# Performance work log

Hardware: AMD Instinct MI355X
Metric: run time of the kernel (lower is better)

## Reference

```python
import jax, jax.numpy as jnp
import numpy as np

B, D_IN, D_OUT, M, KS = 8192, 4096, 4096, 32, 256
CHUNK = D_IN // M  # 128; d_input divisible by m -> all chunks equal width


def setup_inputs() -> dict:
    key = jax.random.key(0)
    k1, k2, k3, k4 = jax.random.split(key, 4)
    x = jax.random.normal(k1, (B, D_IN), dtype=jnp.float32)
    W = jax.random.normal(k2, (M, CHUNK, KS), dtype=jnp.float32) * (1.0 / np.sqrt(CHUNK))
    b = jax.random.normal(k3, (M, KS), dtype=jnp.float32) * 0.01
    idx = jax.random.randint(k4, (M, D_OUT), 0, KS)
    return {"x": x, "W": W, "b": b, "idx": idx}


def reference(x, W, b, idx):
    # x: (B, d_input); W: (m, chunk, ks); b: (m, ks); idx: (m, d_output)
    Bn = x.shape[0]
    m, chunk, ks = W.shape
    d_out = idx.shape[1]
    xs = x.reshape(Bn, m, chunk)
    # All m small Linears as one batched GEMM -> (m, B, ks)
    proj = jnp.einsum('bmc,mck->mbk', xs, W) + b[:, None, :]
    # Gather per-chunk codebook outputs and accumulate without materializing (B, m, d_out)
    def step(acc, inputs):
        p, ix = inputs  # p: (B, ks), ix: (d_out,)
        return acc + p[:, ix], None
    init = jnp.zeros((Bn, d_out), dtype=x.dtype)
    out, _ = jax.lax.scan(step, init, (proj, idx))
    return out
```

## Files before the change

### kernel.cpp

```cpp
#include <hip/hip_runtime.h>
#include <cstdint>


#define M_CB   32
#define CHUNK_C 128
#define KS_K   256
#define DIN    4096

#define GLOAD_LDS16(gp, lp)                                                      \
  __builtin_amdgcn_global_load_lds(                                              \
      (const __attribute__((address_space(1))) void*)(gp),                       \
      (__attribute__((address_space(3))) void*)(lp), 16, 0, 0)

__global__ __launch_bounds__(256, 3)
void k1_gemm(const float* __restrict__ x, const float* __restrict__ W,
             const float* __restrict__ bias, float* __restrict__ proj,
             int b0_chunk, int Bc) {
  const int t  = threadIdx.x;
  const int bq = t & 15;
  const int g  = t >> 4;
  const int m  = blockIdx.y;
  const int bb = blockIdx.x * 64;

  __shared__ float xs[32 * 68];
  __shared__ float Wl[32 * 256];

  float4 acc[16];
#pragma unroll
  for (int a = 0; a < 4; ++a) {
    float4 bv = *(const float4*)&bias[m * KS_K + g * 16 + 4 * a];
    acc[4 * a + 0] = make_float4(bv.x, bv.x, bv.x, bv.x);
    acc[4 * a + 1] = make_float4(bv.y, bv.y, bv.y, bv.y);
    acc[4 * a + 2] = make_float4(bv.z, bv.z, bv.z, bv.z);
    acc[4 * a + 3] = make_float4(bv.w, bv.w, bv.w, bv.w);
  }

  const float* xg = x + (size_t)(b0_chunk + bb) * DIN + m * CHUNK_C;
  const float* Wg = W + (size_t)m * CHUNK_C * KS_K;

  for (int cc = 0; cc < 4; ++cc) {
    __syncthreads();
    {
      const float* src = Wg + (size_t)(cc * 32) * KS_K;
      const int wb = (t & ~63);
#pragma unroll
      for (int i = 0; i < 8; ++i) {
        const int C = t + 256 * i;
        GLOAD_LDS16(src + 4 * C, (char*)Wl + (size_t)(wb + 256 * i) * 16);
      }
    }
#pragma unroll
    for (int i = 0; i < 2; ++i) {
      const int f = t + 256 * i;
      const int b = f >> 3, cq = f & 7;
      float4 v = *(const float4*)&xg[(size_t)b * DIN + cc * 32 + 4 * cq];
      xs[(4 * cq + 0) * 68 + b] = v.x;
      xs[(4 * cq + 1) * 68 + b] = v.y;
      xs[(4 * cq + 2) * 68 + b] = v.z;
      xs[(4 * cq + 3) * 68 + b] = v.w;
    }
    asm volatile("s_waitcnt vmcnt(0)" ::: "memory");
    __syncthreads();

#define FMA4(J, S)                                      \
  {                                                     \
    acc[J].x = fmaf(xq.x, (S), acc[J].x);               \
    acc[J].y = fmaf(xq.y, (S), acc[J].y);               \
    acc[J].z = fmaf(xq.z, (S), acc[J].z);               \
    acc[J].w = fmaf(xq.w, (S), acc[J].w);               \
  }
#pragma unroll 2
    for (int c = 0; c < 32; ++c) {
      float4 xq = *(float4*)&xs[c * 68 + 4 * bq];
      float4 w0 = *(float4*)&Wl[c * 256 + g * 16 + 0];
      float4 w1 = *(float4*)&Wl[c * 256 + g * 16 + 4];
      float4 w2 = *(float4*)&Wl[c * 256 + g * 16 + 8];
      float4 w3 = *(float4*)&Wl[c * 256 + g * 16 + 12];
      FMA4(0, w0.x)  FMA4(1, w0.y)  FMA4(2, w0.z)  FMA4(3, w0.w)
      FMA4(4, w1.x)  FMA4(5, w1.y)  FMA4(6, w1.z)  FMA4(7, w1.w)
      FMA4(8, w2.x)  FMA4(9, w2.y)  FMA4(10, w2.z) FMA4(11, w2.w)
      FMA4(12, w3.x) FMA4(13, w3.y) FMA4(14, w3.z) FMA4(15, w3.w)
    }
#undef FMA4
  }

#pragma unroll
  for (int j = 0; j < 16; ++j) {
    const int k = g * 16 + j;
    *(float4*)&proj[((size_t)m * KS_K + k) * Bc + bb + 4 * bq] = acc[j];
  }
}

__global__ __launch_bounds__(512, 2)
void k2_gather(const float* __restrict__ proj, const int* __restrict__ idx,
               float* __restrict__ out, int b0_chunk, int Bc, int D_out) {
  const int t  = threadIdx.x;
  const int q  = t & 7;
  const int g  = t >> 3;
  const int b0 = blockIdx.x * 32;
  const int dbase = blockIdx.y * 2048 + g * 32;

  __shared__ float pb[2][8192];

  float4 acc[32];
#pragma unroll
  for (int j = 0; j < 32; ++j) acc[j] = make_float4(0.f, 0.f, 0.f, 0.f);

  const int q16 = q << 4;
  const int* ixp = idx + dbase;

#define STAGE(MM, BUF)                                                          \
  {                                                                             \
    const float* src_ = proj + (size_t)(MM)*KS_K * Bc + b0;                     \
    const int wb_ = (t & ~63);                                                  \
    _Pragma("unroll") for (int i_ = 0; i_ < 4; ++i_) {                          \
      const int C_ = t + 512 * i_;              \
      const int k_ = C_ >> 3, qp_ = C_ & 7;                                     \
      GLOAD_LDS16(src_ + (size_t)k_ * Bc + 4 * qp_,                             \
                  (char*)(BUF) + (size_t)(wb_ + 512 * i_) * 16);                \
    }                                                                           \
  }

  STAGE(0, pb[0]);
  int4 iv[8];
#pragma unroll
  for (int a = 0; a < 8; ++a) iv[a] = *(const int4*)&ixp[4 * a];
  asm volatile("s_waitcnt vmcnt(0)" ::: "memory");
  __syncthreads();

  int cur = 0;
  for (int m = 0; m < M_CB; ++m) {
    int4 ivn[8];
    if (m < M_CB - 1) {
      const int* ixn = ixp + (size_t)(m + 1) * D_out;
#pragma unroll
      for (int a = 0; a < 8; ++a) ivn[a] = *(const int4*)&ixn[4 * a];
      STAGE(m + 1, pb[cur ^ 1]);
    }

    const char* pbase = (const char*)&pb[cur][0] + q16;
#define GSTEP(KV, J)                                                            \
  {                                                                             \
    const float4 v_ = *(const float4*)(pbase + ((KV) << 7));                    \
    acc[J].x += v_.x; acc[J].y += v_.y; acc[J].z += v_.z; acc[J].w += v_.w;     \
  }
#pragma unroll
    for (int a = 0; a < 8; ++a) {
      GSTEP(iv[a].x, 4 * a + 0)
      GSTEP(iv[a].y, 4 * a + 1)
      GSTEP(iv[a].z, 4 * a + 2)
      GSTEP(iv[a].w, 4 * a + 3)
    }
#undef GSTEP
    asm volatile("s_waitcnt vmcnt(0)" ::: "memory");
    __syncthreads();
    if (m < M_CB - 1) {
#pragma unroll
      for (int a = 0; a < 8; ++a) iv[a] = ivn[a];
    }
    cur ^= 1;
  }
#undef STAGE

  float* op = out + (size_t)(b0_chunk + b0 + 4 * q) * D_out + dbase;
#pragma unroll
  for (int a = 0; a < 8; ++a) {
    float4 o0 = make_float4(acc[4*a+0].x, acc[4*a+1].x, acc[4*a+2].x, acc[4*a+3].x);
    float4 o1 = make_float4(acc[4*a+0].y, acc[4*a+1].y, acc[4*a+2].y, acc[4*a+3].y);
    float4 o2 = make_float4(acc[4*a+0].z, acc[4*a+1].z, acc[4*a+2].z, acc[4*a+3].z);
    float4 o3 = make_float4(acc[4*a+0].w, acc[4*a+1].w, acc[4*a+2].w, acc[4*a+3].w);
    *(float4*)(op + 0 * (size_t)D_out + 4 * a) = o0;
    *(float4*)(op + 1 * (size_t)D_out + 4 * a) = o1;
    *(float4*)(op + 2 * (size_t)D_out + 4 * a) = o2;
    *(float4*)(op + 3 * (size_t)D_out + 4 * a) = o3;
  }
}

extern "C" void kernel_launch(void* const* d_in, const int* in_sizes, int n_in,
                              void* d_out, int out_size, void* d_ws, size_t ws_size,
                              hipStream_t stream) {
  const float* x    = (const float*)d_in[0];
  const float* W    = (const float*)d_in[1];
  const float* bias = (const float*)d_in[2];
  const int*   idx  = (const int*)d_in[3];
  float* out  = (float*)d_out;
  float* proj = (float*)d_ws;

  const int B     = in_sizes[0] / DIN;
  const int D_out = in_sizes[3] / M_CB;

  size_t maxBc = ws_size / ((size_t)M_CB * KS_K * sizeof(float));
  int Bc = 4096;
  if ((size_t)Bc > maxBc) Bc = (int)(maxBc & ~(size_t)63);
  if (Bc > B) Bc = B;
  if (Bc < 64) Bc = 64;

  for (int b0 = 0; b0 < B; b0 += Bc) {
    int cb = (B - b0 < Bc) ? (B - b0) : Bc;
    dim3 g1(cb / 64, M_CB);
    k1_gemm<<<g1, 256, 0, stream>>>(x, W, bias, proj, b0, cb);
    dim3 g2(cb / 32, D_out / 2048);
    k2_gather<<<g2, 512, 0, stream>>>(proj, idx, out, b0, cb, D_out);
  }
}
```

Measured before the change: 653.5 us.

## Use split-bf16 MFMA for chunk GEMM and deepen gather prefetch pipeline

The fp32 FMA GEMM is replaced by a bf16 MFMA GEMM that emulates fp32 with a three-term hi/lo split (hi*hi + hi*lo + lo*hi). A new prep kernel converts W into swizzled hi/lo bf16 images, and x is split on the fly into swizzled LDS tiles. The gather kernel moves from double to quad buffering, with partial vmcnt waits and raw barriers so loads overlap the gather. The split trades some accuracy and extra MFMA work for matrix-core throughput, and the deeper buffering doubles LDS use.

```diff
diff --git a/kernel.cpp b/kernel.cpp
--- a/kernel.cpp
+++ b/kernel.cpp
@@ -2,93 +2,161 @@
 #include <cstdint>
 
 
-#define M_CB   32
+#define M_CB    32
 #define CHUNK_C 128
-#define KS_K   256
-#define DIN    4096
+#define KS_K    256
+#define DIN     4096
+
+typedef __attribute__((ext_vector_type(8))) short  bf16x8;
+typedef __attribute__((ext_vector_type(4))) float  f32x4;
 
 #define GLOAD_LDS16(gp, lp)                                                      \
   __builtin_amdgcn_global_load_lds(                                              \
       (const __attribute__((address_space(1))) void*)(gp),                       \
       (__attribute__((address_space(3))) void*)(lp), 16, 0, 0)
 
-__global__ __launch_bounds__(256, 3)
-void k1_gemm(const float* __restrict__ x, const float* __restrict__ W,
-             const float* __restrict__ bias, float* __restrict__ proj,
-             int b0_chunk, int Bc) {
-  const int t  = threadIdx.x;
-  const int bq = t & 15;
-  const int g  = t >> 4;
+__device__ __forceinline__ ushort f2bf_rne(float f, float* back) {
+  unsigned u = __float_as_uint(f);
+  unsigned r = (u + 0x7FFFu + ((u >> 16) & 1u)) >> 16;
+  *back = __uint_as_float(r << 16);
+  return (ushort)r;
+}
+
+__global__ void k0_prep(const float* __restrict__ W, ushort* __restrict__ Whp,
+                        ushort* __restrict__ Wlp) {
+  const int tid = blockIdx.x * 256 + threadIdx.x;
+  const int ch = tid & 3;
+  const int k  = (tid >> 2) & 255;
+  const int cs = (tid >> 10) & 3;
+  const int m  = tid >> 12;
+  const float* src = W + ((size_t)m * CHUNK_C + cs * 32 + ch * 8) * KS_K + k;
+  union { int4 i4; ushort us[8]; } uh, ul;
+#pragma unroll
+  for (int j = 0; j < 8; ++j) {
+    float f = src[(size_t)j * KS_K];
+    float back, d2;
+    uh.us[j] = f2bf_rne(f, &back);
+    ul.us[j] = f2bf_rne(f - back, &d2);
+  }
+  const size_t img = ((size_t)m * 4 + cs) * 8192;
+  const int off_us = ((k * 64 + ch * 16) ^ ((k & 7) << 4)) >> 1;
+  *(int4*)&Whp[img + off_us] = uh.i4;
+  *(int4*)&Wlp[img + off_us] = ul.i4;
+}
+
+__global__ __launch_bounds__(256, 2)
+void k1_mfma(const float* __restrict__ x, const ushort* __restrict__ Whp,
+             const ushort* __restrict__ Wlp, const float* __restrict__ bias,
+             float* __restrict__ proj, int b0_chunk, int Bc) {
+  const int t    = threadIdx.x;
+  const int lane = t & 63;
+  const int wv   = t >> 6;
+  const int l15  = lane & 15;
+  const int lg   = lane >> 4;
   const int m  = blockIdx.y;
   const int bb = blockIdx.x * 64;
-
-  __shared__ float xs[32 * 68];
-  __shared__ float Wl[32 * 256];
-
-  float4 acc[16];
-#pragma unroll
-  for (int a = 0; a < 4; ++a) {
-    float4 bv = *(const float4*)&bias[m * KS_K + g * 16 + 4 * a];
-    acc[4 * a + 0] = make_float4(bv.x, bv.x, bv.x, bv.x);
-    acc[4 * a + 1] = make_float4(bv.y, bv.y, bv.y, bv.y);
-    acc[4 * a + 2] = make_float4(bv.z, bv.z, bv.z, bv.z);
-    acc[4 * a + 3] = make_float4(bv.w, bv.w, bv.w, bv.w);
-  }
-
-  const float* xg = x + (size_t)(b0_chunk + bb) * DIN + m * CHUNK_C;
-  const float* Wg = W + (size_t)m * CHUNK_C * KS_K;
-
-  for (int cc = 0; cc < 4; ++cc) {
-    __syncthreads();
-    {
-      const float* src = Wg + (size_t)(cc * 32) * KS_K;
-      const int wb = (t & ~63);
-#pragma unroll
-      for (int i = 0; i < 8; ++i) {
-        const int C = t + 256 * i;
-        GLOAD_LDS16(src + 4 * C, (char*)Wl + (size_t)(wb + 256 * i) * 16);
+  const int wb = t & ~63;
+
+  __shared__ ushort wbuf[16384];
+  __shared__ ushort xh[8192];
+  __shared__ ushort xl[8192];
+
+  f32x4 acc[4][4];
+  {
+    const float* bp = bias + m * KS_K + wv * 64 + lg * 4;
+#pragma unroll
+    for (int kt = 0; kt < 4; ++kt) {
+      f32x4 bv = *(const f32x4*)&bp[kt * 16];
+#pragma unroll
+      for (int bt = 0; bt < 4; ++bt) acc[bt][kt] = bv;
+    }
+  }
+
+  const ushort* wh_img = Whp + (size_t)m * 4 * 8192;
+  const ushort* wlo_img = Wlp + (size_t)m * 4 * 8192;
+
+#define STAGE_W(CS)                                                             \
+  {                                                                             \
+    const ushort* wh_cs = wh_img + (size_t)(CS) * 8192;                         \
+    const ushort* wl_cs = wlo_img + (size_t)(CS) * 8192;                        \
+    _Pragma("unroll") for (int i_ = 0; i_ < 8; ++i_) {                          \
+      const int C_ = t + 256 * i_;                                              \
+      const ushort* s_ = (C_ < 1024) ? (wh_cs + C_ * 8) : (wl_cs + (C_ - 1024) * 8); \
+      GLOAD_LDS16(s_, (char*)wbuf + (size_t)(wb + 256 * i_) * 16);              \
+    }                                                                           \
+  }
+
+  const int bloc = t >> 2, c4 = t & 3;
+  const float* xg = x + (size_t)(b0_chunk + bb + bloc) * DIN + m * CHUNK_C + c4 * 32;
+  float4 xv[8];
+#pragma unroll
+  for (int j = 0; j < 8; ++j) xv[j] = *(const float4*)&xg[4 * j];
+
+  STAGE_W(0);
+
+  {
+    union { int4 i4; ushort us[8]; } H[4], L[4];
+#pragma unroll
+    for (int cj = 0; cj < 4; ++cj) {
+#pragma unroll
+      for (int e = 0; e < 8; ++e) {
+        float f = ((const float*)&xv[cj * 2 + (e >> 2)])[e & 3];
+        float back, d2;
+        H[cj].us[e] = f2bf_rne(f, &back);
+        L[cj].us[e] = f2bf_rne(f - back, &d2);
       }
     }
 #pragma unroll
-    for (int i = 0; i < 2; ++i) {
-      const int f = t + 256 * i;
-      const int b = f >> 3, cq = f & 7;
-      float4 v = *(const float4*)&xg[(size_t)b * DIN + cc * 32 + 4 * cq];
-      xs[(4 * cq + 0) * 68 + b] = v.x;
-      xs[(4 * cq + 1) * 68 + b] = v.y;
-      xs[(4 * cq + 2) * 68 + b] = v.z;
-      xs[(4 * cq + 3) * 68 + b] = v.w;
-    }
-    asm volatile("s_waitcnt vmcnt(0)" ::: "memory");
-    __syncthreads();
-
-#define FMA4(J, S)                                      \
-  {                                                     \
-    acc[J].x = fmaf(xq.x, (S), acc[J].x);               \
-    acc[J].y = fmaf(xq.y, (S), acc[J].y);               \
-    acc[J].z = fmaf(xq.z, (S), acc[J].z);               \
-    acc[J].w = fmaf(xq.w, (S), acc[J].w);               \
-  }
-#pragma unroll 2
-    for (int c = 0; c < 32; ++c) {
-      float4 xq = *(float4*)&xs[c * 68 + 4 * bq];
-      float4 w0 = *(float4*)&Wl[c * 256 + g * 16 + 0];
-      float4 w1 = *(float4*)&Wl[c * 256 + g * 16 + 4];
-      float4 w2 = *(float4*)&Wl[c * 256 + g * 16 + 8];
-      float4 w3 = *(float4*)&Wl[c * 256 + g * 16 + 12];
-      FMA4(0, w0.x)  FMA4(1, w0.y)  FMA4(2, w0.z)  FMA4(3, w0.w)
-      FMA4(4, w1.x)  FMA4(5, w1.y)  FMA4(6, w1.z)  FMA4(7, w1.w)
-      FMA4(8, w2.x)  FMA4(9, w2.y)  FMA4(10, w2.z) FMA4(11, w2.w)
-      FMA4(12, w3.x) FMA4(13, w3.y) FMA4(14, w3.z) FMA4(15, w3.w)
-    }
-#undef FMA4
-  }
-
-#pragma unroll
-  for (int j = 0; j < 16; ++j) {
-    const int k = g * 16 + j;
-    *(float4*)&proj[((size_t)m * KS_K + k) * Bc + bb + 4 * bq] = acc[j];
-  }
+    for (int cj = 0; cj < 4; ++cj) {
+      const int ch = c4 * 4 + cj;
+      const int off = bloc * 256 + ((ch ^ (bloc & 7)) << 4);
+      *(int4*)((char*)xh + off) = H[cj].i4;
+      *(int4*)((char*)xl + off) = L[cj].i4;
+    }
+  }
+  asm volatile("s_waitcnt vmcnt(0)" ::: "memory");
+  __syncthreads();
+
+  for (int cs = 0; cs < 4; ++cs) {
+    bf16x8 Ah[4], Al[4];
+#pragma unroll
+    for (int kt = 0; kt < 4; ++kt) {
+      const int k = wv * 64 + kt * 16 + l15;
+      const int off = (k * 64 + lg * 16) ^ ((k & 7) << 4);
+      Ah[kt] = *(const bf16x8*)((const char*)wbuf + off);
+      Al[kt] = *(const bf16x8*)((const char*)wbuf + 16384 + off);
+    }
+#pragma unroll
+    for (int bt = 0; bt < 4; ++bt) {
+      const int b = bt * 16 + l15;
+      const int off = b * 256 + (((cs * 4 + lg) ^ (b & 7)) << 4);
+      bf16x8 Bh = *(const bf16x8*)((const char*)xh + off);
+      bf16x8 Bl = *(const bf16x8*)((const char*)xl + off);
+#pragma unroll
+      for (int kt = 0; kt < 4; ++kt) {
+        acc[bt][kt] = __builtin_amdgcn_mfma_f32_16x16x32_bf16(Ah[kt], Bh, acc[bt][kt], 0, 0, 0);
+        acc[bt][kt] = __builtin_amdgcn_mfma_f32_16x16x32_bf16(Ah[kt], Bl, acc[bt][kt], 0, 0, 0);
+        acc[bt][kt] = __builtin_amdgcn_mfma_f32_16x16x32_bf16(Al[kt], Bh, acc[bt][kt], 0, 0, 0);
+      }
+    }
+    if (cs < 3) {
+      __syncthreads();
+      STAGE_W(cs + 1);
+      asm volatile("s_waitcnt vmcnt(0)" ::: "memory");
+      __syncthreads();
+    }
+  }
+#undef STAGE_W
+
+#pragma unroll
+  for (int bt = 0; bt < 4; ++bt)
+#pragma unroll
+    for (int kt = 0; kt < 4; ++kt)
+#pragma unroll
+      for (int j = 0; j < 4; ++j) {
+        const int row = wv * 64 + kt * 16 + lg * 4 + j;
+        proj[(size_t)(m * KS_K + row) * Bc + bb + bt * 16 + l15] = acc[bt][kt][j];
+      }
 }
 
 __global__ __launch_bounds__(512, 2)
@@ -100,79 +168,92 @@
   const int b0 = blockIdx.x * 32;
   const int dbase = blockIdx.y * 2048 + g * 32;
 
-  __shared__ float pb[2][8192];
-
-  float4 acc[32];
-#pragma unroll
-  for (int j = 0; j < 32; ++j) acc[j] = make_float4(0.f, 0.f, 0.f, 0.f);
+  __shared__ float pb[4][8192];
+
+  f32x4 acc[32];
+#pragma unroll
+  for (int j = 0; j < 32; ++j) acc[j] = (f32x4){0.f, 0.f, 0.f, 0.f};
 
   const int q16 = q << 4;
   const int* ixp = idx + dbase;
+  const int wbk = t & ~63;
 
 #define STAGE(MM, BUF)                                                          \
   {                                                                             \
-    const float* src_ = proj + (size_t)(MM)*KS_K * Bc + b0;                     \
-    const int wb_ = (t & ~63);                                                  \
+    const float* src_ = proj + (size_t)(MM) * KS_K * Bc + b0;                   \
     _Pragma("unroll") for (int i_ = 0; i_ < 4; ++i_) {                          \
-      const int C_ = t + 512 * i_;              \
+      const int C_ = t + 512 * i_;                                              \
       const int k_ = C_ >> 3, qp_ = C_ & 7;                                     \
       GLOAD_LDS16(src_ + (size_t)k_ * Bc + 4 * qp_,                             \
-                  (char*)(BUF) + (size_t)(wb_ + 512 * i_) * 16);                \
-    }                                                                           \
-  }
-
+                  (char*)(BUF) + (size_t)(wbk + 512 * i_) * 16);                \
+    }                                                                           \
+  }
+#define LOADIDX(MM, DST)                                                        \
+  {                                                                             \
+    const int* ix_ = ixp + (size_t)(MM) * D_out;                                \
+    _Pragma("unroll") for (int a_ = 0; a_ < 8; ++a_)                            \
+      (DST)[a_] = *(const int4*)&ix_[4 * a_];                                   \
+  }
+#define GATHER(IVU)                                                             \
+  {                                                                             \
+    _Pragma("unroll") for (int a_ = 0; a_ < 8; ++a_) {                          \
+      const f32x4 v0_ = *(const f32x4*)(pbase + ((IVU)[a_].x << 7));            \
+      const f32x4 v1_ = *(const f32x4*)(pbase + ((IVU)[a_].y << 7));            \
+      const f32x4 v2_ = *(const f32x4*)(pbase + ((IVU)[a_].z << 7));            \
+      const f32x4 v3_ = *(const f32x4*)(pbase + ((IVU)[a_].w << 7));            \
+      acc[4 * a_ + 0] += v0_; acc[4 * a_ + 1] += v1_;                           \
+      acc[4 * a_ + 2] += v2_; acc[4 * a_ + 3] += v3_;                           \
+    }                                                                           \
+  }
+#define K2ITER(MM, IVU, IVL)                                                    \
+  {                                                                             \
+    if ((MM) + 1 < M_CB) LOADIDX((MM) + 1, IVL);                                \
+    __builtin_amdgcn_sched_barrier(0);                                          \
+    if ((MM) + 3 < M_CB) STAGE((MM) + 3, pb[((MM) + 3) & 3]);                   \
+    __builtin_amdgcn_sched_barrier(0);                                          \
+    const char* pbase = (const char*)&pb[(MM) & 3][0] + q16;                    \
+    GATHER(IVU);                                                                \
+    if ((MM) < M_CB - 1) {                                                      \
+      if ((MM) <= M_CB - 4)      { asm volatile("s_waitcnt vmcnt(16)" ::: "memory"); } \
+      else if ((MM) == M_CB - 3) { asm volatile("s_waitcnt vmcnt(12)" ::: "memory"); } \
+      else                       { asm volatile("s_waitcnt vmcnt(8)"  ::: "memory"); } \
+      __builtin_amdgcn_s_barrier();                                             \
+      __builtin_amdgcn_sched_barrier(0);                                        \
+    }                                                                           \
+  }
+
+  int4 iva[8], ivb[8];
   STAGE(0, pb[0]);
-  int4 iv[8];
-#pragma unroll
-  for (int a = 0; a < 8; ++a) iv[a] = *(const int4*)&ixp[4 * a];
-  asm volatile("s_waitcnt vmcnt(0)" ::: "memory");
-  __syncthreads();
-
-  int cur = 0;
-  for (int m = 0; m < M_CB; ++m) {
-    int4 ivn[8];
-    if (m < M_CB - 1) {
-      const int* ixn = ixp + (size_t)(m + 1) * D_out;
-#pragma unroll
-      for (int a = 0; a < 8; ++a) ivn[a] = *(const int4*)&ixn[4 * a];
-      STAGE(m + 1, pb[cur ^ 1]);
-    }
-
-    const char* pbase = (const char*)&pb[cur][0] + q16;
-#define GSTEP(KV, J)                                                            \
-  {                                                                             \
-    const float4 v_ = *(const float4*)(pbase + ((KV) << 7));                    \
-    acc[J].x += v_.x; acc[J].y += v_.y; acc[J].z += v_.z; acc[J].w += v_.w;     \
-  }
-#pragma unroll
-    for (int a = 0; a < 8; ++a) {
-      GSTEP(iv[a].x, 4 * a + 0)
-      GSTEP(iv[a].y, 4 * a + 1)
-      GSTEP(iv[a].z, 4 * a + 2)
-      GSTEP(iv[a].w, 4 * a + 3)
-    }
-#undef GSTEP
-    asm volatile("s_waitcnt vmcnt(0)" ::: "memory");
-    __syncthreads();
-    if (m < M_CB - 1) {
-#pragma unroll
-      for (int a = 0; a < 8; ++a) iv[a] = ivn[a];
-    }
-    cur ^= 1;
-  }
+  __builtin_amdgcn_sched_barrier(0);
+  LOADIDX(0, iva);
+  __builtin_amdgcn_sched_barrier(0);
+  STAGE(1, pb[1]);
+  STAGE(2, pb[2]);
+  asm volatile("s_waitcnt vmcnt(16)" ::: "memory");
+  __builtin_amdgcn_s_barrier();
+  __builtin_amdgcn_sched_barrier(0);
+
+  for (int mm = 0; mm < M_CB; mm += 2) {
+    K2ITER(mm, iva, ivb);
+    K2ITER(mm + 1, ivb, iva);
+  }
+#undef K2ITER
+#undef GATHER
+#undef LOADIDX
 #undef STAGE
 
   float* op = out + (size_t)(b0_chunk + b0 + 4 * q) * D_out + dbase;
 #pragma unroll
   for (int a = 0; a < 8; ++a) {
-    float4 o0 = make_float4(acc[4*a+0].x, acc[4*a+1].x, acc[4*a+2].x, acc[4*a+3].x);
-    float4 o1 = make_float4(acc[4*a+0].y, acc[4*a+1].y, acc[4*a+2].y, acc[4*a+3].y);
-    float4 o2 = make_float4(acc[4*a+0].z, acc[4*a+1].z, acc[4*a+2].z, acc[4*a+3].z);
-    float4 o3 = make_float4(acc[4*a+0].w, acc[4*a+1].w, acc[4*a+2].w, acc[4*a+3].w);
-    *(float4*)(op + 0 * (size_t)D_out + 4 * a) = o0;
-    *(float4*)(op + 1 * (size_t)D_out + 4 * a) = o1;
-    *(float4*)(op + 2 * (size_t)D_out + 4 * a) = o2;
-    *(float4*)(op + 3 * (size_t)D_out + 4 * a) = o3;
+    f32x4 o0, o1, o2, o3;
+    o0[0]=acc[4*a+0][0]; o0[1]=acc[4*a+1][0]; o0[2]=acc[4*a+2][0]; o0[3]=acc[4*a+3][0];
+    o1[0]=acc[4*a+0][1]; o1[1]=acc[4*a+1][1]; o1[2]=acc[4*a+2][1]; o1[3]=acc[4*a+3][1];
+    o2[0]=acc[4*a+0][2]; o2[1]=acc[4*a+1][2]; o2[2]=acc[4*a+2][2]; o2[3]=acc[4*a+3][2];
+    o3[0]=acc[4*a+0][3]; o3[1]=acc[4*a+1][3]; o3[2]=acc[4*a+2][3]; o3[3]=acc[4*a+3][3];
+    *(f32x4*)(op + 0 * (size_t)D_out + 4 * a) = o0;
+    *(f32x4*)(op + 1 * (size_t)D_out + 4 * a) = o1;
+    *(f32x4*)(op + 2 * (size_t)D_out + 4 * a) = o2;
+    *(f32x4*)(op + 3 * (size_t)D_out + 4 * a) = o3;
   }
 }
 
@@ -183,22 +264,27 @@
   const float* W    = (const float*)d_in[1];
   const float* bias = (const float*)d_in[2];
   const int*   idx  = (const int*)d_in[3];
-  float* out  = (float*)d_out;
-  float* proj = (float*)d_ws;
+  float* out = (float*)d_out;
+
+  ushort* Whp = (ushort*)d_ws;
+  ushort* Wlp = (ushort*)((char*)d_ws + (2u << 20));
+  float*  proj = (float*)((char*)d_ws + (4u << 20));
 
   const int B     = in_sizes[0] / DIN;
   const int D_out = in_sizes[3] / M_CB;
 
-  size_t maxBc = ws_size / ((size_t)M_CB * KS_K * sizeof(float));
+  size_t maxBc = (ws_size - (4u << 20)) / ((size_t)M_CB * KS_K * sizeof(float));
   int Bc = 4096;
   if ((size_t)Bc > maxBc) Bc = (int)(maxBc & ~(size_t)63);
   if (Bc > B) Bc = B;
   if (Bc < 64) Bc = 64;
 
+  k0_prep<<<512, 256, 0, stream>>>(W, Whp, Wlp);
+
   for (int b0 = 0; b0 < B; b0 += Bc) {
     int cb = (B - b0 < Bc) ? (B - b0) : Bc;
     dim3 g1(cb / 64, M_CB);
-    k1_gemm<<<g1, 256, 0, stream>>>(x, W, bias, proj, b0, cb);
+    k1_mfma<<<g1, 256, 0, stream>>>(x, Whp, Wlp, bias, proj, b0, cb);
     dim3 g2(cb / 32, D_out / 2048);
     k2_gather<<<g2, 512, 0, stream>>>(proj, idx, out, b0, cb, D_out);
   }
```

Measured after the change: 1.599 ms. +144.6%, slower.
